# Kernel optimization log

Hardware: AMD Instinct MI355X
Metric: run time of the kernel (lower is better)

Reference implementation:

```python
import jax, jax.numpy as jnp
import numpy as np

N_EXP = 8
TOP_K = 2
CAPACITY_FACTOR = 1.25


def setup_inputs() -> dict:
    key = jax.random.key(0)
    ks = jax.random.split(key, 5)
    B, T, D = 4, 1024, 1024
    H = 4 * D
    E = N_EXP
    x = jax.random.normal(ks[0], (B, T, D), jnp.float32)
    gate_w = jax.random.normal(ks[1], (D, E), jnp.float32) * 0.02
    c_fc = jax.random.normal(ks[2], (E, D, H), jnp.float32) * 0.02
    fc_bias = jnp.zeros((E, 1, H), jnp.float32)
    c_proj = jax.random.normal(ks[3], (E, H, D), jnp.float32) * 0.02
    proj_bias = jnp.zeros((E, 1, D), jnp.float32)
    return dict(x=x, gate_w=gate_w, c_fc=c_fc, fc_bias=fc_bias,
                c_proj=c_proj, proj_bias=proj_bias)


def reference(x, gate_w, c_fc, fc_bias, c_proj, proj_bias):
    B, T, D = x.shape
    n = B * T
    E, k = N_EXP, TOP_K
    cap = int(CAPACITY_FACTOR * n * k / E)  # expert capacity

    xt = x.reshape(n, D)

    # ---- Router ----
    logits = xt @ gate_w                                   # [n, E]
    top_logits, top_idx = jax.lax.top_k(logits, k)         # [n, k]
    # softmax over only the top-k experts (others set to -inf)
    masked = jnp.full_like(logits, -jnp.inf)
    masked = masked.at[jnp.arange(n)[:, None], top_idx].set(top_logits)
    router_probs = jax.nn.softmax(masked, axis=-1)         # [n, E]

    exp_mask = jax.nn.one_hot(top_idx, E, dtype=jnp.int32)  # [n, k, E]
    exp_mask = jnp.transpose(exp_mask, (1, 0, 2))           # [k, n, E]

    # rank of each token within its expert's batch (k=0 choices first)
    exp_rank = jnp.cumsum(exp_mask.reshape(k * n, E), axis=0) - 1
    exp_rank = exp_rank.reshape(k, n, E)

    # drop tokens exceeding capacity
    exp_mask = exp_mask * (exp_rank < cap).astype(jnp.int32)
    used_capacity = jnp.sum(exp_mask, axis=(0, 1))          # [E]

    exp_rank = jnp.sum(exp_mask * exp_rank, axis=-1)        # [k, n] slot index

    exp_weights = exp_mask.astype(x.dtype) * router_probs[None]  # [k, n, E]
    rank_oh = jax.nn.one_hot(exp_rank, cap, dtype=x.dtype)        # [k, n, cap]

    # combine weights [n, E, cap]
    cb_weight = jnp.einsum('kne,knc->nec', exp_weights, rank_oh)
    sec_mask = (cb_weight != 0).astype(x.dtype)             # dispatch mask

    # ---- Dispatch: one-hot matmul -> per-expert batches ----
    exp_batches = jnp.einsum('nec,nd->ecd', sec_mask, xt)   # [E, cap, D]

    # ---- Expert MLP (batched GEMMs, exact GELU, dropout=0/eval) ----
    h = jnp.einsum('ecd,edh->ech', exp_batches, c_fc) + fc_bias
    h = jax.nn.gelu(h, approximate=False)
    exp_out = jnp.einsum('ech,ehd->ecd', h, c_proj) + proj_bias  # [E, cap, D]

    # ---- Combine ----
    out = jnp.einsum('nec,ecd->nd', cb_weight, exp_out)     # [n, D]
    return out.reshape(B, T, D)
```

## Files before the change

kernel.cpp:

```cpp
#include <hip/hip_runtime.h>
#include <hip/hip_bf16.h>

typedef unsigned short u16;
typedef unsigned int u32;

#define N_TOK 4096
#define DIM   1024
#define HID   4096
#define N_EXP 8
#define CAP   1280

typedef short short8 __attribute__((ext_vector_type(8)));
typedef float f32x4 __attribute__((ext_vector_type(4)));

__device__ __forceinline__ u16 bf16rne(float f) {
    u32 u = __float_as_uint(f);
    u32 r = u + 0x7FFFu + ((u >> 16) & 1u);
    return (u16)(r >> 16);
}
__device__ __forceinline__ float bf2f(u16 h) {
    return __uint_as_float(((u32)h) << 16);
}

__global__ void router_kernel(const float* __restrict__ x,
                              const float* __restrict__ gw,
                              int* __restrict__ r_eidx,
                              float* __restrict__ r_w) {
    const int wave = threadIdx.x >> 6, lane = threadIdx.x & 63;
    const int t = blockIdx.x * 4 + wave;
    const float* xr = x + (size_t)t * DIM;
    float acc[8];
#pragma unroll
    for (int e = 0; e < 8; e++) acc[e] = 0.f;
#pragma unroll 4
    for (int i = 0; i < DIM / 64; i++) {
        int d = i * 64 + lane;
        float xv = xr[d];
        const float4* g = (const float4*)(gw + (size_t)d * 8);
        float4 g0 = g[0], g1 = g[1];
        acc[0] += xv * g0.x; acc[1] += xv * g0.y;
        acc[2] += xv * g0.z; acc[3] += xv * g0.w;
        acc[4] += xv * g1.x; acc[5] += xv * g1.y;
        acc[6] += xv * g1.z; acc[7] += xv * g1.w;
    }
#pragma unroll
    for (int e = 0; e < 8; e++) {
#pragma unroll
        for (int off = 32; off > 0; off >>= 1)
            acc[e] += __shfl_xor(acc[e], off, 64);
    }
    if (lane == 0) {
        int e0 = 0; float l0 = acc[0];
#pragma unroll
        for (int e = 1; e < 8; e++) if (acc[e] > l0) { l0 = acc[e]; e0 = e; }
        int e1 = -1; float l1 = -1e30f;
#pragma unroll
        for (int e = 0; e < 8; e++) if (e != e0 && acc[e] > l1) { l1 = acc[e]; e1 = e; }
        float z = __expf(l1 - l0);
        float inv = 1.f / (1.f + z);
        r_eidx[t] = e0; r_eidx[N_TOK + t] = e1;
        r_w[t] = inv;   r_w[N_TOK + t] = z * inv;
    }
}

__global__ void assign_kernel(const int* __restrict__ r_eidx,
                              int* __restrict__ assign_slot,
                              int* __restrict__ token_for_slot) {
    const int tid = threadIdx.x;
    __shared__ int wtot[8][16];
    __shared__ int wbase[8][16];
    for (int i = tid; i < N_EXP * CAP; i += 1024) token_for_slot[i] = -1;

    int le[8], lr[8], cnt[8];
#pragma unroll
    for (int e = 0; e < 8; e++) cnt[e] = 0;
#pragma unroll
    for (int j = 0; j < 8; j++) {
        int e = r_eidx[tid * 8 + j];
        le[j] = e;
        int r = 0;
#pragma unroll
        for (int e2 = 0; e2 < 8; e2++)
            if (e == e2) { r = cnt[e2]; cnt[e2] = r + 1; }
        lr[j] = r;
    }
    const int lane = tid & 63, wv = tid >> 6;
    int excl[8];
#pragma unroll
    for (int e = 0; e < 8; e++) {
        int v = cnt[e], inc = v;
#pragma unroll
        for (int off = 1; off < 64; off <<= 1) {
            int u = __shfl_up(inc, off, 64);
            if (lane >= off) inc += u;
        }
        excl[e] = inc - v;
        if (lane == 63) wtot[e][wv] = inc;
    }
    __syncthreads();
    if (tid < 8) {
        int s = 0;
        for (int w = 0; w < 16; w++) { wbase[tid][w] = s; s += wtot[tid][w]; }
    }
    __syncthreads();
#pragma unroll
    for (int j = 0; j < 8; j++) {
        int i = tid * 8 + j;
        int e = le[j];
        int b = 0;
#pragma unroll
        for (int e2 = 0; e2 < 8; e2++)
            if (e == e2) b = wbase[e2][wv] + excl[e2];
        int rank = b + lr[j];
        int tok = i & (N_TOK - 1);
        if (rank < CAP) {
            assign_slot[i] = rank;
            token_for_slot[e * CAP + rank] = tok;
        } else {
            assign_slot[i] = -1;
        }
    }
}

__global__ void gather_kernel(const float* __restrict__ x,
                              const int* __restrict__ token_for_slot,
                              u16* __restrict__ exp_batches) {
    const int s = blockIdx.x;
    const int tok = token_for_slot[s];
    const int d = threadIdx.x * 4;
    ushort4 o;
    if (tok >= 0) {
        float4 v = *(const float4*)(x + (size_t)tok * DIM + d);
        o = make_ushort4(bf16rne(v.x), bf16rne(v.y), bf16rne(v.z), bf16rne(v.w));
    } else {
        o = make_ushort4(0, 0, 0, 0);
    }
    *(ushort4*)(exp_batches + (size_t)s * DIM + d) = o;
}

#define BM 128
#define BN 128
#define BKT 64
#define LDT 72

template <bool DO_GELU>
__global__ __launch_bounds__(256, 2) void moe_gemm(
    const u16* __restrict__ A, const float* __restrict__ Bw,
    const float* __restrict__ bias, u16* __restrict__ C,
    int M, int N, int K) {
    __shared__ __align__(16) u16 As[BM * LDT];
    __shared__ __align__(16) u16 Bs[BN * LDT];

    const int e = blockIdx.z;
    A    += (size_t)e * M * K;
    Bw   += (size_t)e * K * N;
    bias += (size_t)e * N;
    C    += (size_t)e * M * N;

    const int tid = threadIdx.x;
    const int lane = tid & 63, wave = tid >> 6;
    const int wr = (wave >> 1) * 64, wc = (wave & 1) * 64;
    const int row0 = blockIdx.y * BM, col0 = blockIdx.x * BN;

    f32x4 acc[4][4];
#pragma unroll
    for (int i = 0; i < 4; i++)
#pragma unroll
        for (int j = 0; j < 4; j++) acc[i][j] = (f32x4){0.f, 0.f, 0.f, 0.f};

    const int ar = tid >> 1, ah = (tid & 1) * 32;
    const int bkg = tid >> 5, bng = (tid & 31) * 4;

    for (int kt = 0; kt < K; kt += BKT) {
        const u16* Ag = A + (size_t)(row0 + ar) * K + kt + ah;
#pragma unroll
        for (int c = 0; c < 4; c++) {
            uint4 v = *(const uint4*)(Ag + c * 8);
            *(uint4*)(As + ar * LDT + ah + c * 8) = v;
        }
#pragma unroll
        for (int p = 0; p < 2; p++) {
            int g = bkg + p * 8;
            const float* Bg = Bw + (size_t)(kt + g * 4) * N + col0 + bng;
            float4 f0 = *(const float4*)(Bg);
            float4 f1 = *(const float4*)(Bg + N);
            float4 f2 = *(const float4*)(Bg + 2 * (size_t)N);
            float4 f3 = *(const float4*)(Bg + 3 * (size_t)N);
            const float* q0 = (const float*)&f0;
            const float* q1 = (const float*)&f1;
            const float* q2 = (const float*)&f2;
            const float* q3 = (const float*)&f3;
#pragma unroll
            for (int j = 0; j < 4; j++) {
                u32 lo = (u32)bf16rne(q0[j]) | ((u32)bf16rne(q1[j]) << 16);
                u32 hi = (u32)bf16rne(q2[j]) | ((u32)bf16rne(q3[j]) << 16);
                uint2 w2; w2.x = lo; w2.y = hi;
                *(uint2*)(Bs + (bng + j) * LDT + g * 4) = w2;
            }
        }
        __syncthreads();
#pragma unroll
        for (int ks = 0; ks < 2; ks++) {
            const int krd = ks * 32 + (lane >> 4) * 8;
            const int rrd = lane & 15;
            short8 af[4], bfr[4];
#pragma unroll
            for (int i = 0; i < 4; i++)
                af[i] = *(const short8*)(As + (wr + i * 16 + rrd) * LDT + krd);
#pragma unroll
            for (int j = 0; j < 4; j++)
                bfr[j] = *(const short8*)(Bs + (wc + j * 16 + rrd) * LDT + krd);
#pragma unroll
            for (int i = 0; i < 4; i++)
#pragma unroll
                for (int j = 0; j < 4; j++)
                    acc[i][j] = __builtin_amdgcn_mfma_f32_16x16x32_bf16(
                        af[i], bfr[j], acc[i][j], 0, 0, 0);
        }
        __syncthreads();
    }
    const int cr = (lane >> 4) * 4;
    const int cc = lane & 15;
#pragma unroll
    for (int j = 0; j < 4; j++) {
        const int col = col0 + wc + j * 16 + cc;
        const float bv = bias[col];
#pragma unroll
        for (int i = 0; i < 4; i++) {
#pragma unroll
            for (int r = 0; r < 4; r++) {
                int row = row0 + wr + i * 16 + cr + r;
                float v = acc[i][j][r] + bv;
                if (DO_GELU) v = 0.5f * v * (1.0f + erff(v * 0.70710678118f));
                C[(size_t)row * N + col] = bf16rne(v);
            }
        }
    }
}

__global__ void combine_kernel(const int* __restrict__ r_eidx,
                               const float* __restrict__ r_w,
                               const int* __restrict__ assign_slot,
                               const u16* __restrict__ exp_out,
                               float* __restrict__ out) {
    const int t = blockIdx.x;
    const int d = threadIdx.x * 4;
    const int e0 = r_eidx[t], e1 = r_eidx[N_TOK + t];
    const float w0 = r_w[t], w1 = r_w[N_TOK + t];
    const int s0 = assign_slot[t], s1 = assign_slot[N_TOK + t];
    float v0 = 0.f, v1 = 0.f, v2 = 0.f, v3 = 0.f;
    if (s0 >= 0) {
        const u16* p = exp_out + ((size_t)e0 * CAP + s0) * DIM + d;
        ushort4 q = *(const ushort4*)p;
        v0 += w0 * bf2f(q.x); v1 += w0 * bf2f(q.y);
        v2 += w0 * bf2f(q.z); v3 += w0 * bf2f(q.w);
    }
    if (s1 >= 0) {
        const u16* p = exp_out + ((size_t)e1 * CAP + s1) * DIM + d;
        ushort4 q = *(const ushort4*)p;
        v0 += w1 * bf2f(q.x); v1 += w1 * bf2f(q.y);
        v2 += w1 * bf2f(q.z); v3 += w1 * bf2f(q.w);
    }
    float4 o; o.x = v0; o.y = v1; o.z = v2; o.w = v3;
    *(float4*)(out + (size_t)t * DIM + d) = o;
}

extern "C" void kernel_launch(void* const* d_in, const int* in_sizes, int n_in,
                              void* d_out, int out_size, void* d_ws, size_t ws_size,
                              hipStream_t stream) {
    const float* x         = (const float*)d_in[0];
    const float* gate_w    = (const float*)d_in[1];
    const float* c_fc      = (const float*)d_in[2];
    const float* fc_bias   = (const float*)d_in[3];
    const float* c_proj    = (const float*)d_in[4];
    const float* proj_bias = (const float*)d_in[5];
    float* out = (float*)d_out;
    char* ws = (char*)d_ws;

    int*   r_eidx         = (int*)(ws + 0);
    float* r_w            = (float*)(ws + 32768);
    int*   assign_slot    = (int*)(ws + 65536);
    int*   token_for_slot = (int*)(ws + 98304);
    u16*   exp_batches    = (u16*)(ws + 139264);
    u16*   h              = (u16*)(ws + 21110784);
    u16*   exp_out        = (u16*)(ws + 104996864);

    router_kernel<<<N_TOK / 4, 256, 0, stream>>>(x, gate_w, r_eidx, r_w);
    assign_kernel<<<1, 1024, 0, stream>>>(r_eidx, assign_slot, token_for_slot);
    gather_kernel<<<N_EXP * CAP, 256, 0, stream>>>(x, token_for_slot, exp_batches);
    moe_gemm<true><<<dim3(HID / BN, CAP / BM, N_EXP), 256, 0, stream>>>(
        exp_batches, c_fc, fc_bias, h, CAP, HID, DIM);
    moe_gemm<false><<<dim3(DIM / BN, CAP / BM, N_EXP), 256, 0, stream>>>(
        h, c_proj, proj_bias, exp_out, CAP, DIM, HID);
    combine_kernel<<<N_TOK, 256, 0, stream>>>(r_eidx, r_w, assign_slot, exp_out, out);
}
```

Before: 687.3 us.

## Pre-transpose weights to bf16 and stream GEMM tiles via global_load_lds with swizzle

Adds a transpose-and-convert kernel that writes each expert's fp32 weight matrix into a bf16 [N,K] buffer before each GEMM. The GEMM then loads both A and B tiles straight into LDS with global_load_lds, using an XOR-swizzled layout in place of the padded rows. This removes the per-tile fp32-to-bf16 conversion, the strided B stores, and the register round-trip inside the GEMM main loop. The cost is an extra full pass over the weights each call: an fp32 read plus a bf16 write.

```diff
diff --git a/kernel.cpp b/kernel.cpp
--- a/kernel.cpp
+++ b/kernel.cpp
@@ -21,6 +21,10 @@
 __device__ __forceinline__ float bf2f(u16 h) {
     return __uint_as_float(((u32)h) << 16);
 }
+
+#define GLDS(gp, lp) __builtin_amdgcn_global_load_lds( \
+    (const __attribute__((address_space(1))) void*)(gp), \
+    (__attribute__((address_space(3))) void*)(lp), 16, 0, 0)
 
 __global__ void router_kernel(const float* __restrict__ x,
                               const float* __restrict__ gw,
@@ -138,29 +142,56 @@
     *(ushort4*)(exp_batches + (size_t)s * DIM + d) = o;
 }
 
-#define BM 128
-#define BN 128
-#define BKT 64
-#define LDT 72
+__global__ __launch_bounds__(256) void transpose_cvt(
+    const float* __restrict__ in, u16* __restrict__ out, int R, int C) {
+    __shared__ float t[64][65];
+    const int ez = blockIdx.z;
+    in  += (size_t)ez * R * C;
+    out += (size_t)ez * R * C;
+    const int row0 = blockIdx.y * 64, col0 = blockIdx.x * 64;
+    const int tid = threadIdx.x;
+    {
+        const int r = tid >> 2, cq = (tid & 3) * 16;
+        const float* p = in + (size_t)(row0 + r) * C + col0 + cq;
+        float4 v0 = ((const float4*)p)[0];
+        float4 v1 = ((const float4*)p)[1];
+        float4 v2 = ((const float4*)p)[2];
+        float4 v3 = ((const float4*)p)[3];
+        float tmp[16] = {v0.x, v0.y, v0.z, v0.w, v1.x, v1.y, v1.z, v1.w,
+                         v2.x, v2.y, v2.z, v2.w, v3.x, v3.y, v3.z, v3.w};
+#pragma unroll
+        for (int j = 0; j < 16; j++) t[r][cq + j] = tmp[j];
+    }
+    __syncthreads();
+    {
+        const int oc = tid >> 2, h4 = (tid & 3) * 16;
+        u16 o[16];
+#pragma unroll
+        for (int i = 0; i < 16; i++) o[i] = bf16rne(t[h4 + i][oc]);
+        u16* q = out + (size_t)(col0 + oc) * R + row0 + h4;
+        *(uint4*)q = *(const uint4*)&o[0];
+        *(uint4*)(q + 8) = *(const uint4*)&o[8];
+    }
+}
 
 template <bool DO_GELU>
 __global__ __launch_bounds__(256, 2) void moe_gemm(
-    const u16* __restrict__ A, const float* __restrict__ Bw,
+    const u16* __restrict__ A, const u16* __restrict__ Bt,
     const float* __restrict__ bias, u16* __restrict__ C,
     int M, int N, int K) {
-    __shared__ __align__(16) u16 As[BM * LDT];
-    __shared__ __align__(16) u16 Bs[BN * LDT];
+    __shared__ __align__(16) u16 As[128 * 64];
+    __shared__ __align__(16) u16 Bs[128 * 64];
 
     const int e = blockIdx.z;
     A    += (size_t)e * M * K;
-    Bw   += (size_t)e * K * N;
+    Bt   += (size_t)e * N * K;
     bias += (size_t)e * N;
     C    += (size_t)e * M * N;
 
     const int tid = threadIdx.x;
     const int lane = tid & 63, wave = tid >> 6;
     const int wr = (wave >> 1) * 64, wc = (wave & 1) * 64;
-    const int row0 = blockIdx.y * BM, col0 = blockIdx.x * BN;
+    const int row0 = blockIdx.y * 128, col0 = blockIdx.x * 128;
 
     f32x4 acc[4][4];
 #pragma unroll
@@ -168,48 +199,35 @@
 #pragma unroll
         for (int j = 0; j < 4; j++) acc[i][j] = (f32x4){0.f, 0.f, 0.f, 0.f};
 
-    const int ar = tid >> 1, ah = (tid & 1) * 32;
-    const int bkg = tid >> 5, bng = (tid & 31) * 4;
-
-    for (int kt = 0; kt < K; kt += BKT) {
-        const u16* Ag = A + (size_t)(row0 + ar) * K + kt + ah;
-#pragma unroll
-        for (int c = 0; c < 4; c++) {
-            uint4 v = *(const uint4*)(Ag + c * 8);
-            *(uint4*)(As + ar * LDT + ah + c * 8) = v;
-        }
-#pragma unroll
-        for (int p = 0; p < 2; p++) {
-            int g = bkg + p * 8;
-            const float* Bg = Bw + (size_t)(kt + g * 4) * N + col0 + bng;
-            float4 f0 = *(const float4*)(Bg);
-            float4 f1 = *(const float4*)(Bg + N);
-            float4 f2 = *(const float4*)(Bg + 2 * (size_t)N);
-            float4 f3 = *(const float4*)(Bg + 3 * (size_t)N);
-            const float* q0 = (const float*)&f0;
-            const float* q1 = (const float*)&f1;
-            const float* q2 = (const float*)&f2;
-            const float* q3 = (const float*)&f3;
-#pragma unroll
-            for (int j = 0; j < 4; j++) {
-                u32 lo = (u32)bf16rne(q0[j]) | ((u32)bf16rne(q1[j]) << 16);
-                u32 hi = (u32)bf16rne(q2[j]) | ((u32)bf16rne(q3[j]) << 16);
-                uint2 w2; w2.x = lo; w2.y = hi;
-                *(uint2*)(Bs + (bng + j) * LDT + g * 4) = w2;
-            }
-        }
+    const int srow = lane >> 3;
+    const int swz = ((lane & 7) ^ srow) * 8;
+    const u16* Ab = A + (size_t)(row0 + wave * 32 + srow) * K + swz;
+    const u16* Bb = Bt + (size_t)(col0 + wave * 32 + srow) * K + swz;
+    u16* Asw = As + (wave * 4) * 512;
+    u16* Bsw = Bs + (wave * 4) * 512;
+
+    const int rrd = lane & 15, qrd = lane >> 4;
+    const int sw = rrd & 7;
+
+    for (int kt = 0; kt < K; kt += 64) {
+#pragma unroll
+        for (int i = 0; i < 4; i++)
+            GLDS(Ab + (size_t)(i * 8) * K + kt, Asw + i * 512);
+#pragma unroll
+        for (int i = 0; i < 4; i++)
+            GLDS(Bb + (size_t)(i * 8) * K + kt, Bsw + i * 512);
         __syncthreads();
 #pragma unroll
         for (int ks = 0; ks < 2; ks++) {
-            const int krd = ks * 32 + (lane >> 4) * 8;
-            const int rrd = lane & 15;
+            const int kc = ks * 4 + qrd;
+            const int krd = (kc ^ sw) * 8;
             short8 af[4], bfr[4];
 #pragma unroll
             for (int i = 0; i < 4; i++)
-                af[i] = *(const short8*)(As + (wr + i * 16 + rrd) * LDT + krd);
+                af[i] = *(const short8*)(As + (wr + i * 16 + rrd) * 64 + krd);
 #pragma unroll
             for (int j = 0; j < 4; j++)
-                bfr[j] = *(const short8*)(Bs + (wc + j * 16 + rrd) * LDT + krd);
+                bfr[j] = *(const short8*)(Bs + (wc + j * 16 + rrd) * 64 + krd);
 #pragma unroll
             for (int i = 0; i < 4; i++)
 #pragma unroll
@@ -281,16 +299,24 @@
     float* r_w            = (float*)(ws + 32768);
     int*   assign_slot    = (int*)(ws + 65536);
     int*   token_for_slot = (int*)(ws + 98304);
-    u16*   exp_batches    = (u16*)(ws + 139264);
-    u16*   h              = (u16*)(ws + 21110784);
-    u16*   exp_out        = (u16*)(ws + 104996864);
+    u16*   exp_batches    = (u16*)(ws + 163840);
+    u16*   h              = (u16*)(ws + 21135360);
+    u16*   exp_out        = (u16*)(ws + 105021440);
+    u16*   Bt             = (u16*)(ws + 125992960);
 
     router_kernel<<<N_TOK / 4, 256, 0, stream>>>(x, gate_w, r_eidx, r_w);
     assign_kernel<<<1, 1024, 0, stream>>>(r_eidx, assign_slot, token_for_slot);
     gather_kernel<<<N_EXP * CAP, 256, 0, stream>>>(x, token_for_slot, exp_batches);
-    moe_gemm<true><<<dim3(HID / BN, CAP / BM, N_EXP), 256, 0, stream>>>(
-        exp_batches, c_fc, fc_bias, h, CAP, HID, DIM);
-    moe_gemm<false><<<dim3(DIM / BN, CAP / BM, N_EXP), 256, 0, stream>>>(
-        h, c_proj, proj_bias, exp_out, CAP, DIM, HID);
+
+    transpose_cvt<<<dim3(HID / 64, DIM / 64, N_EXP), 256, 0, stream>>>(
+        c_fc, Bt, DIM, HID);
+    moe_gemm<true><<<dim3(HID / 128, CAP / 128, N_EXP), 256, 0, stream>>>(
+        exp_batches, Bt, fc_bias, h, CAP, HID, DIM);
+
+    transpose_cvt<<<dim3(DIM / 64, HID / 64, N_EXP), 256, 0, stream>>>(
+        c_proj, Bt, HID, DIM);
+    moe_gemm<false><<<dim3(DIM / 128, CAP / 128, N_EXP), 256, 0, stream>>>(
+        h, Bt, proj_bias, exp_out, CAP, DIM, HID);
+
     combine_kernel<<<N_TOK, 256, 0, stream>>>(r_eidx, r_w, assign_slot, exp_out, out);
 }
```

Result: faster. 584.3 us (-15.0%).
